# Kernel optimization log

Measured on AMD Instinct MI355X. Metric: run time of the kernel, lower is better.

## Reference

```python
import jax, jax.numpy as jnp
import numpy as np

DIM = 1024
NUM_HEADS = 16
HEAD_DIM = DIM // NUM_HEADS
EPS = 1e-6


def rmsnorm(x, scale):
    # normalize over last dim (head_dim)
    ms = jnp.mean(x * x, axis=-1, keepdims=True)
    return scale * (x * jax.lax.rsqrt(ms + EPS))


def setup_inputs() -> dict:
    key = jax.random.key(0)
    ks = jax.random.split(key, 12)
    B, Nx, Nc = 2, 2048, 256
    std = 1.0 / np.sqrt(DIM)
    return {
        "x": jax.random.normal(ks[0], (B, Nx, DIM), jnp.float32),
        "c": jax.random.normal(ks[1], (B, Nc, DIM), jnp.float32),
        "w_qkv_x": jax.random.normal(ks[2], (DIM, 3 * DIM), jnp.float32) * std,
        "b_qkv_x": jnp.zeros((3 * DIM,), jnp.float32),
        "w_qkv_c": jax.random.normal(ks[3], (DIM, 3 * DIM), jnp.float32) * std,
        "b_qkv_c": jnp.zeros((3 * DIM,), jnp.float32),
        "s_q_x": jnp.ones((HEAD_DIM,), jnp.float32),
        "s_k_x": jnp.ones((HEAD_DIM,), jnp.float32),
        "s_q_c": jnp.ones((HEAD_DIM,), jnp.float32),
        "s_k_c": jnp.ones((HEAD_DIM,), jnp.float32),
        "w_proj_x": jax.random.normal(ks[4], (DIM, DIM), jnp.float32) * std,
        "b_proj_x": jnp.zeros((DIM,), jnp.float32),
        "w_proj_c": jax.random.normal(ks[5], (DIM, DIM), jnp.float32) * std,
        "b_proj_c": jnp.zeros((DIM,), jnp.float32),
    }


def reference(x, c, w_qkv_x, b_qkv_x, w_qkv_c, b_qkv_c,
              s_q_x, s_k_x, s_q_c, s_k_c,
              w_proj_x, b_proj_x, w_proj_c, b_proj_c):
    B, Nx, C = x.shape
    Nc = c.shape[1]
    H, D = NUM_HEADS, HEAD_DIM

    def split_qkv(t, w, b, n):
        qkv = (t @ w + b).reshape(B, n, 3, H, D)
        qkv = jnp.transpose(qkv, (2, 0, 3, 1, 4))  # [3, B, H, n, D]
        return qkv[0], qkv[1], qkv[2]

    q_x, k_x, v_x = split_qkv(x, w_qkv_x, b_qkv_x, Nx)
    q_c, k_c, v_c = split_qkv(c, w_qkv_c, b_qkv_c, Nc)

    q = jnp.concatenate([rmsnorm(q_x, s_q_x), rmsnorm(q_c, s_q_c)], axis=2)
    k = jnp.concatenate([rmsnorm(k_x, s_k_x), rmsnorm(k_c, s_k_c)], axis=2)
    v = jnp.concatenate([v_x, v_c], axis=2)

    scale = 1.0 / jnp.sqrt(jnp.asarray(D, q.dtype))
    scores = jnp.einsum("bhqd,bhkd->bhqk", q, k) * scale
    attn = jax.nn.softmax(scores, axis=-1)
    out = jnp.einsum("bhqk,bhkd->bhqd", attn, v)  # [B, H, Nx+Nc, D]
    out = jnp.transpose(out, (0, 2, 1, 3)).reshape(B, Nx + Nc, C)

    x_out = out[:, :Nx] @ w_proj_x + b_proj_x
    c_out = out[:, Nx:] @ w_proj_c + b_proj_c
    return x_out, c_out
```

## Files before the change

### kernel.cpp

```cpp
#include <hip/hip_runtime.h>
#include <stdint.h>

typedef __attribute__((ext_vector_type(4))) float  f32x4;
typedef __attribute__((ext_vector_type(8))) short  s16x8;
typedef __attribute__((ext_vector_type(4))) short  s16x4;

constexpr int kDIM = 1024;
constexpr int kD   = 64;
constexpr int kNT  = 2304;

static __device__ __forceinline__ short f2bf(float f) {
  union { float f; uint32_t i; } x; x.f = f;
  uint32_t r = x.i + 0x7fffu + ((x.i >> 16) & 1u);
  return (short)(r >> 16);
}
static __device__ __forceinline__ uint32_t cvtpk(float lo, float hi) {
  uint32_t r;
  asm volatile("v_cvt_pk_bf16_f32 %0, %1, %2" : "=v"(r) : "v"(lo), "v"(hi));
  return r;
}
static __device__ __forceinline__ void gll16(const short* g, short* l) {
  __builtin_amdgcn_global_load_lds((const __attribute__((address_space(1))) void*)g,
                                   (__attribute__((address_space(3))) void*)l, 16, 0, 0);
}
#define FENCE() asm volatile("" ::: "memory")
#define WAITV8() asm volatile("s_waitcnt vmcnt(8)" ::: "memory")
#define WAITV4() asm volatile("s_waitcnt vmcnt(4)" ::: "memory")
#define WAITV0() asm volatile("s_waitcnt vmcnt(0)" ::: "memory")

__global__ __launch_bounds__(256) void k_cast2(const float* __restrict__ x,
                                               short* __restrict__ xb,
                                               const float* __restrict__ c,
                                               short* __restrict__ cb, int nxb) {
  int b = blockIdx.x;
  const float* in = x; short* out = xb;
  if (b >= nxb) { in = c; out = cb; b -= nxb; }
  int i = (b * 256 + threadIdx.x) * 4;
  f32x4 v = *(const f32x4*)(in + i);
  s16x4 o; o[0] = f2bf(v[0]); o[1] = f2bf(v[1]); o[2] = f2bf(v[2]); o[3] = f2bf(v[3]);
  *(s16x4*)(out + i) = o;
}

__global__ __launch_bounds__(256) void k_tcast2(const float* __restrict__ W0,
                                                short* __restrict__ Wt0,
                                                const float* __restrict__ W1,
                                                short* __restrict__ Wt1,
                                                int K, int N) {
  const float* W = blockIdx.z ? W1 : W0;
  short* Wt = blockIdx.z ? Wt1 : Wt0;
  __shared__ float tile[32][33];
  int n0 = blockIdx.x * 32, k0 = blockIdx.y * 32;
  int tx = threadIdx.x, ty = threadIdx.y;
#pragma unroll
  for (int i2 = 0; i2 < 4; ++i2) {
    int r = ty + 8 * i2;
    tile[r][tx] = W[(size_t)(k0 + r) * N + n0 + tx];
  }
  __syncthreads();
#pragma unroll
  for (int i2 = 0; i2 < 4; ++i2) {
    int r = ty + 8 * i2;
    Wt[(size_t)(n0 + r) * K + k0 + tx] = f2bf(tile[tx][r]);
  }
}

__global__ __launch_bounds__(256, 2) void k_gemm(
    const short* A0, const short* Wt0, const float* bias0,
    const float* sq0, const float* sk0,
    const short* A1, const short* Wt1, const float* bias1,
    const float* sq1, const float* sk1,
    short* outq, short* outk, short* outvt,
    float* outp0, float* outp1,
    int rpbs0, int arstride0, int aoff0, int posoff0,
    int rpbs1, int arstride1, int aoff1, int posoff1,
    int ybreak, int epi, int nx) {
  __shared__ __align__(16) short As[2][8192];
  __shared__ __align__(16) short Bs[2][8192];
  const int t = threadIdx.x;
  const int lane = t & 63, w = t >> 6;
  const int g = lane >> 4, r15 = lane & 15;
  const int wm = w >> 1, wn = w & 1;

  int lin = blockIdx.x;
  int xcd = lin & 7, kk = lin >> 3;
  int by = (xcd & 3) * 9 + kk % 9;
  int bx = (xcd >> 2) * (nx >> 1) + kk / 9;

  const short* A; const short* Wt; const float* bias;
  const float* sq; const float* sk; float* outp;
  int rpbs, arstride, aoff, posoff, my;
  if (by < ybreak) {
    A = A0; Wt = Wt0; bias = bias0; sq = sq0; sk = sk0; outp = outp0;
    rpbs = rpbs0; arstride = arstride0; aoff = aoff0; posoff = posoff0; my = by;
  } else {
    A = A1; Wt = Wt1; bias = bias1; sq = sq1; sk = sk1; outp = outp1;
    rpbs = rpbs1; arstride = arstride1; aoff = aoff1; posoff = posoff1; my = by - ybreak;
  }
  const int m0 = my * 128, n0 = bx * 128;

  const short* aptr[4]; const short* bptr[4];
  int wofs[4];
#pragma unroll
  for (int it = 0; it < 4; ++it) {
    int slot = t + 256 * it;
    int row = slot >> 3, gp = slot & 7;
    int gl = gp ^ (row & 7);
    int i = m0 + row;
    int arow = (i >> rpbs) * arstride + aoff + (i & ((1 << rpbs) - 1));
    aptr[it] = A + (size_t)arow * kDIM + 8 * gl;
    bptr[it] = Wt + (size_t)(n0 + row) * kDIM + 8 * gl;
    wofs[it] = (256 * it + 64 * w) * 8;
  }

  f32x4 acc[4][4] = {};

  auto STAGE = [&](short* Asd, short* Bsd) {
#pragma unroll
    for (int it = 0; it < 4; ++it) {
      gll16(aptr[it], Asd + wofs[it]);
      gll16(bptr[it], Bsd + wofs[it]);
      aptr[it] += 64; bptr[it] += 64;
    }
  };

  auto kstep = [&](const short* Ab, const short* Bb, short* Asd, short* Bsd,
                   bool last, bool pref) {
    if (last) WAITV0(); else WAITV8();
    __builtin_amdgcn_s_barrier();
    FENCE();
#pragma unroll
    for (int ks = 0; ks < 2; ++ks) {
      s16x8 af[4], bfr[4];
#pragma unroll
      for (int mf = 0; mf < 4; ++mf) {
        int row = wm * 64 + mf * 16 + r15;
        af[mf] = *(const s16x8*)(Ab + row * 64 + (((g + 4 * ks) ^ (row & 7)) * 8));
      }
#pragma unroll
      for (int nf = 0; nf < 4; ++nf) {
        int row = wn * 64 + nf * 16 + r15;
        bfr[nf] = *(const s16x8*)(Bb + row * 64 + (((g + 4 * ks) ^ (row & 7)) * 8));
      }
#pragma unroll
      for (int mf = 0; mf < 4; ++mf)
#pragma unroll
        for (int nf = 0; nf < 4; ++nf)
          acc[mf][nf] = __builtin_amdgcn_mfma_f32_16x16x32_bf16(af[mf], bfr[nf], acc[mf][nf], 0, 0, 0);
    }
    FENCE();
    __builtin_amdgcn_s_barrier();
    FENCE();
    if (pref) STAGE(Asd, Bsd);
  };

  STAGE(&As[0][0], &Bs[0][0]);
  STAGE(&As[1][0], &Bs[1][0]);
  for (int pp = 0; pp < 8; ++pp) {
    kstep(&As[0][0], &Bs[0][0], &As[0][0], &Bs[0][0], false,   pp < 7);
    kstep(&As[1][0], &Bs[1][0], &As[1][0], &Bs[1][0], pp == 7, pp < 7);
  }

  const int rpbm = (1 << rpbs) - 1;
  if (epi == 1) {
#pragma unroll
    for (int mf = 0; mf < 4; ++mf)
#pragma unroll
      for (int nf = 0; nf < 4; ++nf) {
        int i = m0 + wm * 64 + mf * 16 + 4 * g;
        int j = n0 + wn * 64 + nf * 16 + r15;
        f32x4 v = acc[mf][nf];
        float bj = bias[j];
#pragma unroll
        for (int rg = 0; rg < 4; ++rg)
          outp[(size_t)(i + rg) * 1024 + j] = v[rg] + bj;
      }
    return;
  }
  const int eblk = (n0 + wn * 64) >> 10;
  const int hh = ((n0 + wn * 64) >> 6) & 15;
  if (eblk == 2) {
#pragma unroll
    for (int mf = 0; mf < 4; ++mf)
#pragma unroll
      for (int nf = 0; nf < 4; ++nf) {
        int i = m0 + wm * 64 + mf * 16 + 4 * g;
        int j = n0 + wn * 64 + nf * 16 + r15;
        f32x4 v = acc[mf][nf];
        float bj = bias[j];
        int d = j & 63;
        int b = i >> rpbs;
        int pos = (i & rpbm) + posoff;
        int pg = (pos & ~63) | (pos & 32) | (((pos >> 2) & 3) << 3) |
                 (((pos >> 4) & 1) << 2) | (pos & 3);
        size_t base = ((size_t)((b * 16 + hh) * 64 + d)) * kNT + pg;
        s16x4 o;
        o[0] = f2bf(v[0] + bj); o[1] = f2bf(v[1] + bj);
        o[2] = f2bf(v[2] + bj); o[3] = f2bf(v[3] + bj);
        *(s16x4*)(outvt + base) = o;
      }
  } else {
    const float* sv = (eblk == 0) ? sq : sk;
    short* dstb = (eblk == 0) ? outq : outk;
    const float post = (eblk == 0) ? 0.125f * 1.44269504f : 1.0f;
    float sl[4], bj4[4];
#pragma unroll
    for (int nf = 0; nf < 4; ++nf) {
      bj4[nf] = bias[n0 + wn * 64 + nf * 16 + r15];
      sl[nf] = sv[nf * 16 + r15] * post;
    }
#pragma unroll
    for (int mf = 0; mf < 4; ++mf) {
      float vb[4][4];
#pragma unroll
      for (int nf = 0; nf < 4; ++nf)
#pragma unroll
        for (int rg = 0; rg < 4; ++rg)
          vb[nf][rg] = acc[mf][nf][rg] + bj4[nf];
#pragma unroll
      for (int rg = 0; rg < 4; ++rg) {
        float ss = vb[0][rg] * vb[0][rg];
        ss = __builtin_fmaf(vb[1][rg], vb[1][rg], ss);
        ss = __builtin_fmaf(vb[2][rg], vb[2][rg], ss);
        ss = __builtin_fmaf(vb[3][rg], vb[3][rg], ss);
        ss += __shfl_xor(ss, 1); ss += __shfl_xor(ss, 2);
        ss += __shfl_xor(ss, 4); ss += __shfl_xor(ss, 8);
        float f = rsqrtf(ss * (1.f / 64.f) + 1e-6f);
        int i = m0 + wm * 64 + mf * 16 + 4 * g + rg;
        int b = i >> rpbs;
        int pos = (i & rpbm) + posoff;
        short* dst = dstb + ((size_t)((b * 16 + hh) * kNT + pos)) * 64;
#pragma unroll
        for (int nf = 0; nf < 4; ++nf)
          dst[nf * 16 + r15] = f2bf(vb[nf][rg] * f * sl[nf]);
      }
    }
  }
}

__global__ __launch_bounds__(256, 3) void k_attn(
    const short* __restrict__ Q, const short* __restrict__ K,
    const short* __restrict__ Vt, short* __restrict__ Ao) {
  __shared__ __align__(16) short S[16384];
  const int t = threadIdx.x;
  const int lane = t & 63, w = t >> 6;
  const int g = lane >> 4, r15 = lane & 15;
  const int lin = blockIdx.x;
  const int idx = lin >> 3;
  const int bh = (lin & 7) * 4 + idx / 18;
  const int q0 = (idx % 18) * 128;

  s16x8 qf[2][2];
#pragma unroll
  for (int qi = 0; qi < 2; ++qi) {
    const short* qrow = Q + ((size_t)bh * kNT + q0 + 32 * w + 16 * qi + r15) * kD;
    qf[qi][0] = *(const s16x8*)(qrow + 8 * g);
    qf[qi][1] = *(const s16x8*)(qrow + 32 + 8 * g);
  }

  const short* kptr[2]; const short* vptr[2];
  int sb[2];
#pragma unroll
  for (int it = 0; it < 2; ++it) {
    int slot = t + 256 * it;
    int row = slot >> 3, gp = slot & 7;
    int gl = gp ^ (row & 7);
    kptr[it] = K + ((size_t)bh * kNT + row) * kD + 8 * gl;
    vptr[it] = Vt + ((size_t)bh * kD + row) * kNT + 8 * gl;
    sb[it] = (256 * it + 64 * w) * 8;
  }

  int ko[2][4], vo[2][4];
#pragma unroll
  for (int a = 0; a < 2; ++a)
#pragma unroll
    for (int rf = 0; rf < 4; ++rf) {
      int row = 16 * rf + r15;
      ko[a][rf] = row * 64 + (((g + 4 * a) ^ (row & 7)) * 8);
      vo[a][rf] = row * 64 + (((4 * a + g) ^ (row & 7)) * 8);
    }

  s16x8 onesf;
#pragma unroll
  for (int j = 0; j < 8; ++j) onesf[j] = (short)0x3F80;

  f32x4 ot0[4] = {}, ot1[4] = {};
  f32x4 ls0 = {}, ls1 = {};
  short* Kb0 = S;          short* Kb1 = S + 4096;
  short* Vb0 = S + 8192;   short* Vb1 = S + 12288;

  auto STAGE = [&](short* kst, short* vst) {
#pragma unroll
    for (int it = 0; it < 2; ++it) {
      gll16(kptr[it], kst + sb[it]);
      kptr[it] += 64 * kD;
    }
#pragma unroll
    for (int it = 0; it < 2; ++it) {
      gll16(vptr[it], vst + sb[it]);
      vptr[it] += 64;
    }
  };

  auto tile = [&](const short* Kb, const short* Vb, short* kst, short* vst,
                  bool last, bool pref) {
    if (last) WAITV0(); else WAITV4();
    __builtin_amdgcn_s_barrier();
    FENCE();
    f32x4 st0[4] = {}, st1[4] = {};
    __builtin_amdgcn_s_setprio(1);
#pragma unroll
    for (int a = 0; a < 2; ++a) {
#pragma unroll
      for (int rf = 0; rf < 4; ++rf) {
        s16x8 kf = *(const s16x8*)(Kb + ko[a][rf]);
        st0[rf] = __builtin_amdgcn_mfma_f32_16x16x32_bf16(kf, qf[0][a], st0[rf], 0, 0, 0);
        st1[rf] = __builtin_amdgcn_mfma_f32_16x16x32_bf16(kf, qf[1][a], st1[rf], 0, 0, 0);
      }
    }
    __builtin_amdgcn_s_setprio(0);
    float pv0[4][4], pv1[4][4];
#pragma unroll
    for (int rf = 0; rf < 4; ++rf)
#pragma unroll
      for (int j = 0; j < 4; ++j) {
        pv0[rf][j] = __builtin_amdgcn_exp2f(st0[rf][j]);
        pv1[rf][j] = __builtin_amdgcn_exp2f(st1[rf][j]);
      }
    s16x8 pf0[2], pf1[2];
#pragma unroll
    for (int c = 0; c < 2; ++c) {
      union { uint32_t u[4]; s16x8 v; } a, b;
      a.u[0] = cvtpk(pv0[2 * c][0], pv0[2 * c][1]);
      a.u[1] = cvtpk(pv0[2 * c][2], pv0[2 * c][3]);
      a.u[2] = cvtpk(pv0[2 * c + 1][0], pv0[2 * c + 1][1]);
      a.u[3] = cvtpk(pv0[2 * c + 1][2], pv0[2 * c + 1][3]);
      pf0[c] = a.v;
      b.u[0] = cvtpk(pv1[2 * c][0], pv1[2 * c][1]);
      b.u[1] = cvtpk(pv1[2 * c][2], pv1[2 * c][3]);
      b.u[2] = cvtpk(pv1[2 * c + 1][0], pv1[2 * c + 1][1]);
      b.u[3] = cvtpk(pv1[2 * c + 1][2], pv1[2 * c + 1][3]);
      pf1[c] = b.v;
    }
    __builtin_amdgcn_s_setprio(1);
#pragma unroll
    for (int mf = 0; mf < 4; ++mf)
#pragma unroll
      for (int c = 0; c < 2; ++c) {
        s16x8 vf = *(const s16x8*)(Vb + vo[c][mf]);
        ot0[mf] = __builtin_amdgcn_mfma_f32_16x16x32_bf16(vf, pf0[c], ot0[mf], 0, 0, 0);
        ot1[mf] = __builtin_amdgcn_mfma_f32_16x16x32_bf16(vf, pf1[c], ot1[mf], 0, 0, 0);
      }
#pragma unroll
    for (int c = 0; c < 2; ++c) {
      ls0 = __builtin_amdgcn_mfma_f32_16x16x32_bf16(onesf, pf0[c], ls0, 0, 0, 0);
      ls1 = __builtin_amdgcn_mfma_f32_16x16x32_bf16(onesf, pf1[c], ls1, 0, 0, 0);
    }
    __builtin_amdgcn_s_setprio(0);
    FENCE();
    __builtin_amdgcn_s_barrier();
    FENCE();
    if (pref) STAGE(kst, vst);
  };

  STAGE(Kb0, Vb0);
  STAGE(Kb1, Vb1);
  for (int pp = 0; pp < 18; ++pp) {
    tile(Kb0, Vb0, Kb0, Vb0, false,    pp < 17);
    tile(Kb1, Vb1, Kb1, Vb1, pp == 17, pp < 17);
  }

  float rl0 = 1.f / ls0[0], rl1 = 1.f / ls1[0];

  __syncthreads();
  float* Os = (float*)S;
#pragma unroll
  for (int mf = 0; mf < 4; ++mf)
#pragma unroll
    for (int rg = 0; rg < 4; ++rg) {
      int d = 16 * mf + 4 * g + rg;
      int R0 = 32 * w + r15, R1 = 32 * w + 16 + r15;
      Os[R0 * 64 + (d ^ ((r15 & 7) << 3))] = ot0[mf][rg] * rl0;
      Os[R1 * 64 + (d ^ ((r15 & 7) << 3))] = ot1[mf][rg] * rl1;
    }
  __syncthreads();
  {
    int b = bh >> 4, h = bh & 15;
#pragma unroll
    for (int rep = 0; rep < 2; ++rep) {
      int idx = t + 256 * rep;
      int q = idx >> 2, c4 = idx & 3;
      float vals[16];
#pragma unroll
      for (int i = 0; i < 4; ++i) {
        f32x4 rd = *(const f32x4*)&Os[q * 64 + (((c4 * 16 + 4 * i) ^ ((q & 7) << 3)))];
        vals[4 * i + 0] = rd[0]; vals[4 * i + 1] = rd[1];
        vals[4 * i + 2] = rd[2]; vals[4 * i + 3] = rd[3];
      }
      union { uint32_t u[4]; s16x8 v; } o0, o1;
      o0.u[0] = cvtpk(vals[0], vals[1]);   o0.u[1] = cvtpk(vals[2], vals[3]);
      o0.u[2] = cvtpk(vals[4], vals[5]);   o0.u[3] = cvtpk(vals[6], vals[7]);
      o1.u[0] = cvtpk(vals[8], vals[9]);   o1.u[1] = cvtpk(vals[10], vals[11]);
      o1.u[2] = cvtpk(vals[12], vals[13]); o1.u[3] = cvtpk(vals[14], vals[15]);
      short* dst = Ao + ((size_t)b * kNT + q0 + q) * kDIM + h * kD + c4 * 16;
      *(s16x8*)dst = o0.v;
      *(s16x8*)(dst + 8) = o1.v;
    }
  }
}

extern "C" void kernel_launch(void* const* d_in, const int* in_sizes, int n_in,
                              void* d_out, int out_size, void* d_ws, size_t ws_size,
                              hipStream_t stream) {
  const float* x   = (const float*)d_in[0];
  const float* c   = (const float*)d_in[1];
  const float* wqx = (const float*)d_in[2];
  const float* bqx = (const float*)d_in[3];
  const float* wqc = (const float*)d_in[4];
  const float* bqc = (const float*)d_in[5];
  const float* sqx = (const float*)d_in[6];
  const float* skx = (const float*)d_in[7];
  const float* sqc = (const float*)d_in[8];
  const float* skc = (const float*)d_in[9];
  const float* wpx = (const float*)d_in[10];
  const float* bpx = (const float*)d_in[11];
  const float* wpc = (const float*)d_in[12];
  const float* bpc = (const float*)d_in[13];
  float* out = (float*)d_out;

  char* p = (char*)d_ws;
  short* xb   = (short*)p; p += (size_t)4096 * 1024 * 2;
  short* cb   = (short*)p; p += (size_t)512 * 1024 * 2;
  short* wqxt = (short*)p; p += (size_t)3072 * 1024 * 2;
  short* wqct = (short*)p; p += (size_t)3072 * 1024 * 2;
  short* wpxt = (short*)p; p += (size_t)1024 * 1024 * 2;
  short* wpct = (short*)p; p += (size_t)1024 * 1024 * 2;
  short* qb   = (short*)p; p += (size_t)32 * 2304 * 64 * 2;
  short* kb   = (short*)p; p += (size_t)32 * 2304 * 64 * 2;
  short* vtb  = (short*)p; p += (size_t)32 * 64 * 2304 * 2;
  short* ao   = (short*)p; p += (size_t)2 * 2304 * 1024 * 2;

  k_cast2<<<4608, 256, 0, stream>>>(x, xb, c, cb, 4096);
  k_tcast2<<<dim3(96, 32, 2), dim3(32, 8), 0, stream>>>(wqx, wqxt, wqc, wqct, 1024, 3072);
  k_tcast2<<<dim3(32, 32, 2), dim3(32, 8), 0, stream>>>(wpx, wpxt, wpc, wpct, 1024, 1024);

  k_gemm<<<864, 256, 0, stream>>>(
      xb, wqxt, bqx, sqx, skx,
      cb, wqct, bqc, sqc, skc,
      qb, kb, vtb, nullptr, nullptr,
      11, 2048, 0, 0,
      8, 256, 0, 2048,
      32, 0, 24);

  k_attn<<<576, 256, 0, stream>>>(qb, kb, vtb, ao);

  k_gemm<<<288, 256, 0, stream>>>(
      ao, wpxt, bpx, nullptr, nullptr,
      ao, wpct, bpc, nullptr, nullptr,
      nullptr, nullptr, nullptr, out, out + (size_t)4096 * 1024,
      11, 2304, 0, 0,
      8, 2304, 2048, 0,
      32, 1, 8);
}
```

Before: 129.4 us.

## Stage GEMM epilogues through LDS for coalesced stores; split attention across 8 waves

The GEMM epilogues (projection output, transposed V, and RMS-normalized Q/K) now write each wave's tile into shared memory with a swizzle, then read it back so that global stores are wide and contiguous. Before, the stores were scattered 2-byte, 8-byte or 4-byte writes. The attention kernel now runs 512 threads per block with one 16-row query fragment per wave instead of two, which halves per-wave registers and the K/V staging per thread. The trade-offs are extra LDS traffic and an lgkmcnt wait in the GEMM, and more waves contending for the same LDS tiles in attention.

```diff
diff --git a/kernel.cpp b/kernel.cpp
--- a/kernel.cpp
+++ b/kernel.cpp
@@ -2,6 +2,7 @@
 #include <stdint.h>
 
 typedef __attribute__((ext_vector_type(4))) float  f32x4;
+typedef __attribute__((ext_vector_type(2))) float  f32x2;
 typedef __attribute__((ext_vector_type(8))) short  s16x8;
 typedef __attribute__((ext_vector_type(4))) short  s16x4;
 
@@ -25,8 +26,10 @@
 }
 #define FENCE() asm volatile("" ::: "memory")
 #define WAITV8() asm volatile("s_waitcnt vmcnt(8)" ::: "memory")
-#define WAITV4() asm volatile("s_waitcnt vmcnt(4)" ::: "memory")
+#define WAITV2() asm volatile("s_waitcnt vmcnt(2)" ::: "memory")
 #define WAITV0() asm volatile("s_waitcnt vmcnt(0)" ::: "memory")
+#define WAITLGKM() do { asm volatile("s_waitcnt lgkmcnt(0)" ::: "memory"); \
+                        __builtin_amdgcn_sched_barrier(0); } while (0)
 
 __global__ __launch_bounds__(256) void k_cast2(const float* __restrict__ x,
                                                short* __restrict__ xb,
@@ -74,8 +77,9 @@
     int rpbs0, int arstride0, int aoff0, int posoff0,
     int rpbs1, int arstride1, int aoff1, int posoff1,
     int ybreak, int epi, int nx) {
-  __shared__ __align__(16) short As[2][8192];
-  __shared__ __align__(16) short Bs[2][8192];
+  __shared__ __align__(16) short SH[32768];
+  short* As0 = SH;          short* As1 = SH + 8192;
+  short* Bs0 = SH + 16384;  short* Bs1 = SH + 24576;
   const int t = threadIdx.x;
   const int lane = t & 63, w = t >> 6;
   const int g = lane >> 4, r15 = lane & 15;
@@ -153,29 +157,44 @@
     if (pref) STAGE(Asd, Bsd);
   };
 
-  STAGE(&As[0][0], &Bs[0][0]);
-  STAGE(&As[1][0], &Bs[1][0]);
+  STAGE(As0, Bs0);
+  STAGE(As1, Bs1);
   for (int pp = 0; pp < 8; ++pp) {
-    kstep(&As[0][0], &Bs[0][0], &As[0][0], &Bs[0][0], false,   pp < 7);
-    kstep(&As[1][0], &Bs[1][0], &As[1][0], &Bs[1][0], pp == 7, pp < 7);
+    kstep(As0, Bs0, As0, Bs0, false,   pp < 7);
+    kstep(As1, Bs1, As1, Bs1, pp == 7, pp < 7);
   }
 
   const int rpbm = (1 << rpbs) - 1;
+  float* Ep = (float*)SH + w * 4096;
+
   if (epi == 1) {
 #pragma unroll
     for (int mf = 0; mf < 4; ++mf)
 #pragma unroll
       for (int nf = 0; nf < 4; ++nf) {
-        int i = m0 + wm * 64 + mf * 16 + 4 * g;
-        int j = n0 + wn * 64 + nf * 16 + r15;
         f32x4 v = acc[mf][nf];
-        float bj = bias[j];
-#pragma unroll
-        for (int rg = 0; rg < 4; ++rg)
-          outp[(size_t)(i + rg) * 1024 + j] = v[rg] + bj;
-      }
+        float bj = bias[n0 + wn * 64 + nf * 16 + r15];
+        int dl = nf * 16 + r15;
+#pragma unroll
+        for (int rg = 0; rg < 4; ++rg) {
+          int r = mf * 16 + 4 * g + rg;
+          Ep[r * 64 + (dl ^ ((r & 15) << 1))] = v[rg] + bj;
+        }
+      }
+    WAITLGKM();
+#pragma unroll
+    for (int p2 = 0; p2 < 16; ++p2) {
+      int r = 4 * p2 + (lane >> 4);
+      int ch = lane & 15;
+      int i = m0 + wm * 64 + r;
+      f32x2 a = *(const f32x2*)&Ep[r * 64 + ((ch * 4) ^ ((r & 15) << 1))];
+      f32x2 b2 = *(const f32x2*)&Ep[r * 64 + ((ch * 4 + 2) ^ ((r & 15) << 1))];
+      f32x4 o; o[0] = a[0]; o[1] = a[1]; o[2] = b2[0]; o[3] = b2[1];
+      *(f32x4*)(outp + (size_t)i * 1024 + n0 + wn * 64 + ch * 4) = o;
+    }
     return;
   }
+
   const int eblk = (n0 + wn * 64) >> 10;
   const int hh = ((n0 + wn * 64) >> 6) & 15;
   if (eblk == 2) {
@@ -183,21 +202,33 @@
     for (int mf = 0; mf < 4; ++mf)
 #pragma unroll
       for (int nf = 0; nf < 4; ++nf) {
-        int i = m0 + wm * 64 + mf * 16 + 4 * g;
-        int j = n0 + wn * 64 + nf * 16 + r15;
         f32x4 v = acc[mf][nf];
-        float bj = bias[j];
-        int d = j & 63;
-        int b = i >> rpbs;
-        int pos = (i & rpbm) + posoff;
-        int pg = (pos & ~63) | (pos & 32) | (((pos >> 2) & 3) << 3) |
-                 (((pos >> 4) & 1) << 2) | (pos & 3);
-        size_t base = ((size_t)((b * 16 + hh) * 64 + d)) * kNT + pg;
-        s16x4 o;
-        o[0] = f2bf(v[0] + bj); o[1] = f2bf(v[1] + bj);
-        o[2] = f2bf(v[2] + bj); o[3] = f2bf(v[3] + bj);
-        *(s16x4*)(outvt + base) = o;
-      }
+        float bj = bias[n0 + wn * 64 + nf * 16 + r15];
+        int dl = nf * 16 + r15;
+#pragma unroll
+        for (int rg = 0; rg < 4; ++rg) {
+          int pin = mf * 16 + 4 * g + rg;
+          int pp2 = (pin & 32) | (((pin >> 2) & 3) << 3) |
+                    (((pin >> 4) & 1) << 2) | (pin & 3);
+          Ep[dl * 64 + (pp2 ^ ((dl & 15) << 1))] = v[rg] + bj;
+        }
+      }
+    WAITLGKM();
+    int i0 = m0 + wm * 64;
+    int b = i0 >> rpbs;
+    int posb = (i0 & rpbm) + posoff;
+#pragma unroll
+    for (int p2 = 0; p2 < 8; ++p2) {
+      int dl = 8 * p2 + (lane >> 3);
+      int ch = lane & 7;
+      union { uint32_t u[4]; s16x8 v; } o;
+#pragma unroll
+      for (int j = 0; j < 4; ++j) {
+        f32x2 rd = *(const f32x2*)&Ep[dl * 64 + ((ch * 8 + 2 * j) ^ ((dl & 15) << 1))];
+        o.u[j] = cvtpk(rd[0], rd[1]);
+      }
+      *(s16x8*)(outvt + ((size_t)((b * 16 + hh) * 64 + dl)) * kNT + posb + ch * 8) = o.v;
+    }
   } else {
     const float* sv = (eblk == 0) ? sq : sk;
     short* dstb = (eblk == 0) ? outq : outk;
@@ -225,19 +256,34 @@
         ss += __shfl_xor(ss, 1); ss += __shfl_xor(ss, 2);
         ss += __shfl_xor(ss, 4); ss += __shfl_xor(ss, 8);
         float f = rsqrtf(ss * (1.f / 64.f) + 1e-6f);
-        int i = m0 + wm * 64 + mf * 16 + 4 * g + rg;
-        int b = i >> rpbs;
-        int pos = (i & rpbm) + posoff;
-        short* dst = dstb + ((size_t)((b * 16 + hh) * kNT + pos)) * 64;
-#pragma unroll
-        for (int nf = 0; nf < 4; ++nf)
-          dst[nf * 16 + r15] = f2bf(vb[nf][rg] * f * sl[nf]);
-      }
-    }
-  }
-}
-
-__global__ __launch_bounds__(256, 3) void k_attn(
+        int r = mf * 16 + 4 * g + rg;
+#pragma unroll
+        for (int nf = 0; nf < 4; ++nf) {
+          int dl = nf * 16 + r15;
+          Ep[r * 64 + (dl ^ ((r & 15) << 1))] = vb[nf][rg] * f * sl[nf];
+        }
+      }
+    }
+    WAITLGKM();
+#pragma unroll
+    for (int p2 = 0; p2 < 8; ++p2) {
+      int r = 8 * p2 + (lane >> 3);
+      int ch = lane & 7;
+      int i = m0 + wm * 64 + r;
+      int b = i >> rpbs;
+      int pos = (i & rpbm) + posoff;
+      union { uint32_t u[4]; s16x8 v; } o;
+#pragma unroll
+      for (int j = 0; j < 4; ++j) {
+        f32x2 rd = *(const f32x2*)&Ep[r * 64 + ((ch * 8 + 2 * j) ^ ((r & 15) << 1))];
+        o.u[j] = cvtpk(rd[0], rd[1]);
+      }
+      *(s16x8*)(dstb + ((size_t)((b * 16 + hh) * kNT + pos)) * 64 + ch * 8) = o.v;
+    }
+  }
+}
+
+__global__ __launch_bounds__(512, 4) void k_attn(
     const short* __restrict__ Q, const short* __restrict__ K,
     const short* __restrict__ Vt, short* __restrict__ Ao) {
   __shared__ __align__(16) short S[16384];
@@ -249,25 +295,17 @@
   const int bh = (lin & 7) * 4 + idx / 18;
   const int q0 = (idx % 18) * 128;
 
-  s16x8 qf[2][2];
-#pragma unroll
-  for (int qi = 0; qi < 2; ++qi) {
-    const short* qrow = Q + ((size_t)bh * kNT + q0 + 32 * w + 16 * qi + r15) * kD;
-    qf[qi][0] = *(const s16x8*)(qrow + 8 * g);
-    qf[qi][1] = *(const s16x8*)(qrow + 32 + 8 * g);
-  }
-
-  const short* kptr[2]; const short* vptr[2];
-  int sb[2];
-#pragma unroll
-  for (int it = 0; it < 2; ++it) {
-    int slot = t + 256 * it;
-    int row = slot >> 3, gp = slot & 7;
-    int gl = gp ^ (row & 7);
-    kptr[it] = K + ((size_t)bh * kNT + row) * kD + 8 * gl;
-    vptr[it] = Vt + ((size_t)bh * kD + row) * kNT + 8 * gl;
-    sb[it] = (256 * it + 64 * w) * 8;
-  }
+  const short* qrow = Q + ((size_t)bh * kNT + q0 + 16 * w + r15) * kD;
+  s16x8 qf0 = *(const s16x8*)(qrow + 8 * g);
+  s16x8 qf1 = *(const s16x8*)(qrow + 32 + 8 * g);
+
+  {
+  }
+  int srow = t >> 3, sgp = t & 7;
+  int sgl = sgp ^ (srow & 7);
+  const short* kptr = K + ((size_t)bh * kNT + srow) * kD + 8 * sgl;
+  const short* vptr = Vt + ((size_t)bh * kD + srow) * kNT + 8 * sgl;
+  const int sb2 = 512 * w;
 
   int ko[2][4], vo[2][4];
 #pragma unroll
@@ -283,63 +321,48 @@
 #pragma unroll
   for (int j = 0; j < 8; ++j) onesf[j] = (short)0x3F80;
 
-  f32x4 ot0[4] = {}, ot1[4] = {};
-  f32x4 ls0 = {}, ls1 = {};
+  f32x4 ot[4] = {};
+  f32x4 ls = {};
   short* Kb0 = S;          short* Kb1 = S + 4096;
   short* Vb0 = S + 8192;   short* Vb1 = S + 12288;
 
   auto STAGE = [&](short* kst, short* vst) {
-#pragma unroll
-    for (int it = 0; it < 2; ++it) {
-      gll16(kptr[it], kst + sb[it]);
-      kptr[it] += 64 * kD;
-    }
-#pragma unroll
-    for (int it = 0; it < 2; ++it) {
-      gll16(vptr[it], vst + sb[it]);
-      vptr[it] += 64;
-    }
+    gll16(kptr, kst + sb2); kptr += 64 * kD;
+    gll16(vptr, vst + sb2); vptr += 64;
   };
 
   auto tile = [&](const short* Kb, const short* Vb, short* kst, short* vst,
                   bool last, bool pref) {
-    if (last) WAITV0(); else WAITV4();
+    if (last) WAITV0(); else WAITV2();
     __builtin_amdgcn_s_barrier();
     FENCE();
-    f32x4 st0[4] = {}, st1[4] = {};
+    f32x4 st[4] = {};
     __builtin_amdgcn_s_setprio(1);
 #pragma unroll
     for (int a = 0; a < 2; ++a) {
+      s16x8 qk = a ? qf1 : qf0;
 #pragma unroll
       for (int rf = 0; rf < 4; ++rf) {
         s16x8 kf = *(const s16x8*)(Kb + ko[a][rf]);
-        st0[rf] = __builtin_amdgcn_mfma_f32_16x16x32_bf16(kf, qf[0][a], st0[rf], 0, 0, 0);
-        st1[rf] = __builtin_amdgcn_mfma_f32_16x16x32_bf16(kf, qf[1][a], st1[rf], 0, 0, 0);
+        st[rf] = __builtin_amdgcn_mfma_f32_16x16x32_bf16(kf, qk, st[rf], 0, 0, 0);
       }
     }
     __builtin_amdgcn_s_setprio(0);
-    float pv0[4][4], pv1[4][4];
+    float pv[4][4];
 #pragma unroll
     for (int rf = 0; rf < 4; ++rf)
 #pragma unroll
-      for (int j = 0; j < 4; ++j) {
-        pv0[rf][j] = __builtin_amdgcn_exp2f(st0[rf][j]);
-        pv1[rf][j] = __builtin_amdgcn_exp2f(st1[rf][j]);
-      }
-    s16x8 pf0[2], pf1[2];
+      for (int j = 0; j < 4; ++j)
+        pv[rf][j] = __builtin_amdgcn_exp2f(st[rf][j]);
+    s16x8 pf[2];
 #pragma unroll
     for (int c = 0; c < 2; ++c) {
-      union { uint32_t u[4]; s16x8 v; } a, b;
-      a.u[0] = cvtpk(pv0[2 * c][0], pv0[2 * c][1]);
-      a.u[1] = cvtpk(pv0[2 * c][2], pv0[2 * c][3]);
-      a.u[2] = cvtpk(pv0[2 * c + 1][0], pv0[2 * c + 1][1]);
-      a.u[3] = cvtpk(pv0[2 * c + 1][2], pv0[2 * c + 1][3]);
-      pf0[c] = a.v;
-      b.u[0] = cvtpk(pv1[2 * c][0], pv1[2 * c][1]);
-      b.u[1] = cvtpk(pv1[2 * c][2], pv1[2 * c][3]);
-      b.u[2] = cvtpk(pv1[2 * c + 1][0], pv1[2 * c + 1][1]);
-      b.u[3] = cvtpk(pv1[2 * c + 1][2], pv1[2 * c + 1][3]);
-      pf1[c] = b.v;
+      union { uint32_t u[4]; s16x8 v; } pk;
+      pk.u[0] = cvtpk(pv[2 * c][0], pv[2 * c][1]);
+      pk.u[1] = cvtpk(pv[2 * c][2], pv[2 * c][3]);
+      pk.u[2] = cvtpk(pv[2 * c + 1][0], pv[2 * c + 1][1]);
+      pk.u[3] = cvtpk(pv[2 * c + 1][2], pv[2 * c + 1][3]);
+      pf[c] = pk.v;
     }
     __builtin_amdgcn_s_setprio(1);
 #pragma unroll
@@ -347,14 +370,11 @@
 #pragma unroll
       for (int c = 0; c < 2; ++c) {
         s16x8 vf = *(const s16x8*)(Vb + vo[c][mf]);
-        ot0[mf] = __builtin_amdgcn_mfma_f32_16x16x32_bf16(vf, pf0[c], ot0[mf], 0, 0, 0);
-        ot1[mf] = __builtin_amdgcn_mfma_f32_16x16x32_bf16(vf, pf1[c], ot1[mf], 0, 0, 0);
-      }
-#pragma unroll
-    for (int c = 0; c < 2; ++c) {
-      ls0 = __builtin_amdgcn_mfma_f32_16x16x32_bf16(onesf, pf0[c], ls0, 0, 0, 0);
-      ls1 = __builtin_amdgcn_mfma_f32_16x16x32_bf16(onesf, pf1[c], ls1, 0, 0, 0);
-    }
+        ot[mf] = __builtin_amdgcn_mfma_f32_16x16x32_bf16(vf, pf[c], ot[mf], 0, 0, 0);
+      }
+#pragma unroll
+    for (int c = 0; c < 2; ++c)
+      ls = __builtin_amdgcn_mfma_f32_16x16x32_bf16(onesf, pf[c], ls, 0, 0, 0);
     __builtin_amdgcn_s_setprio(0);
     FENCE();
     __builtin_amdgcn_s_barrier();
@@ -369,7 +389,7 @@
     tile(Kb1, Vb1, Kb1, Vb1, pp == 17, pp < 17);
   }
 
-  float rl0 = 1.f / ls0[0], rl1 = 1.f / ls1[0];
+  float rl = 1.f / ls[0];
 
   __syncthreads();
   float* Os = (float*)S;
@@ -378,33 +398,28 @@
 #pragma unroll
     for (int rg = 0; rg < 4; ++rg) {
       int d = 16 * mf + 4 * g + rg;
-      int R0 = 32 * w + r15, R1 = 32 * w + 16 + r15;
-      Os[R0 * 64 + (d ^ ((r15 & 7) << 3))] = ot0[mf][rg] * rl0;
-      Os[R1 * 64 + (d ^ ((r15 & 7) << 3))] = ot1[mf][rg] * rl1;
+      int R = 16 * w + r15;
+      Os[R * 64 + (d ^ ((r15 & 7) << 3))] = ot[mf][rg] * rl;
     }
   __syncthreads();
   {
     int b = bh >> 4, h = bh & 15;
-#pragma unroll
-    for (int rep = 0; rep < 2; ++rep) {
-      int idx = t + 256 * rep;
-      int q = idx >> 2, c4 = idx & 3;
-      float vals[16];
-#pragma unroll
-      for (int i = 0; i < 4; ++i) {
-        f32x4 rd = *(const f32x4*)&Os[q * 64 + (((c4 * 16 + 4 * i) ^ ((q & 7) << 3)))];
-        vals[4 * i + 0] = rd[0]; vals[4 * i + 1] = rd[1];
-        vals[4 * i + 2] = rd[2]; vals[4 * i + 3] = rd[3];
-      }
-      union { uint32_t u[4]; s16x8 v; } o0, o1;
-      o0.u[0] = cvtpk(vals[0], vals[1]);   o0.u[1] = cvtpk(vals[2], vals[3]);
-      o0.u[2] = cvtpk(vals[4], vals[5]);   o0.u[3] = cvtpk(vals[6], vals[7]);
-      o1.u[0] = cvtpk(vals[8], vals[9]);   o1.u[1] = cvtpk(vals[10], vals[11]);
-      o1.u[2] = cvtpk(vals[12], vals[13]); o1.u[3] = cvtpk(vals[14], vals[15]);
-      short* dst = Ao + ((size_t)b * kNT + q0 + q) * kDIM + h * kD + c4 * 16;
-      *(s16x8*)dst = o0.v;
-      *(s16x8*)(dst + 8) = o1.v;
-    }
+    int q = t >> 2, c4 = t & 3;
+    float vals[16];
+#pragma unroll
+    for (int i = 0; i < 4; ++i) {
+      f32x4 rd = *(const f32x4*)&Os[q * 64 + (((c4 * 16 + 4 * i) ^ ((q & 7) << 3)))];
+      vals[4 * i + 0] = rd[0]; vals[4 * i + 1] = rd[1];
+      vals[4 * i + 2] = rd[2]; vals[4 * i + 3] = rd[3];
+    }
+    union { uint32_t u[4]; s16x8 v; } o0, o1;
+    o0.u[0] = cvtpk(vals[0], vals[1]);   o0.u[1] = cvtpk(vals[2], vals[3]);
+    o0.u[2] = cvtpk(vals[4], vals[5]);   o0.u[3] = cvtpk(vals[6], vals[7]);
+    o1.u[0] = cvtpk(vals[8], vals[9]);   o1.u[1] = cvtpk(vals[10], vals[11]);
+    o1.u[2] = cvtpk(vals[12], vals[13]); o1.u[3] = cvtpk(vals[14], vals[15]);
+    short* dst = Ao + ((size_t)b * kNT + q0 + q) * kDIM + h * kD + c4 * 16;
+    *(s16x8*)dst = o0.v;
+    *(s16x8*)(dst + 8) = o1.v;
   }
 }
 
@@ -451,7 +466,7 @@
       8, 256, 0, 2048,
       32, 0, 24);
 
-  k_attn<<<576, 256, 0, stream>>>(qb, kb, vtb, ao);
+  k_attn<<<576, 512, 0, stream>>>(qb, kb, vtb, ao);
 
   k_gemm<<<288, 256, 0, stream>>>(
       ao, wpxt, bpx, nullptr, nullptr,
```

After: 130.1 us. No clear change (+0.6%).
